# Performance work log

Measured on AMD Instinct MI355X. Metric: run time of the kernel, lower is better.

## Reference

```python
import jax, jax.numpy as jnp
import numpy as np

# dims per init_kwargs / input_specs
N, F_IN, H, C, L = 50000, 128, 128, 40, 4
E = 800000
ALPHA = 0.1   # args.beta -> self.alpha (initial-residual strength)
LAMDA = 0.5   # identity-mapping decay


def setup_inputs() -> dict:
    key = jax.random.key(0)
    ks = jax.random.split(key, 6)
    x = jax.random.normal(ks[0], (N, F_IN), jnp.float32)
    edge_index = jax.random.randint(ks[1], (2, E), 0, N, dtype=jnp.int32)
    s = 1.0 / np.sqrt(H)
    W_in = jax.random.uniform(ks[2], (F_IN, H), jnp.float32, -s, s)
    b_in = jnp.zeros((H,), jnp.float32)
    W_layers = jax.random.uniform(ks[3], (L, H, H), jnp.float32, -s, s)
    W_out = jax.random.uniform(ks[4], (H, C), jnp.float32, -s, s)
    b_out = jnp.zeros((C,), jnp.float32)
    return dict(x=x, edge_index=edge_index, W_in=W_in, b_in=b_in,
                W_layers=W_layers, W_out=W_out, b_out=b_out)


def _gcn_norm(edge_index, n):
    """Symmetric GCN normalization with added self-loops (gcn_norm)."""
    loops = jnp.arange(n, dtype=edge_index.dtype)
    row = jnp.concatenate([edge_index[0], loops])  # destination
    col = jnp.concatenate([edge_index[1], loops])  # source
    deg = jax.ops.segment_sum(jnp.ones(row.shape, jnp.float32), row, num_segments=n)
    dinv = jnp.where(deg > 0, jax.lax.rsqrt(jnp.maximum(deg, 1e-12)), 0.0)
    return row, col, dinv[row] * dinv[col]  # per-edge norm coefficient


def reference(x, edge_index, W_in, b_in, W_layers, W_out, b_out):
    n = x.shape[0]
    row, col, norm = _gcn_norm(edge_index, n)
    # input linear + relu (dropout is identity in eval / p=0)
    h = jax.nn.relu(x @ W_in + b_in)
    h0 = h  # _hidden[0], the initial residual
    # beta_i = log(lamda/(i+1) + 1)
    betas = jnp.log(LAMDA / jnp.arange(1, L + 1, dtype=jnp.float32) + 1.0)

    def layer(h, wb):
        W, beta = wb
        # sparse graph conv: gather-source, scale, scatter-add to dest  [E,H] msgs
        agg = jax.ops.segment_sum(h[col] * norm[:, None], row, num_segments=n)
        support = (1.0 - ALPHA) * agg + ALPHA * h0
        out = beta * (support @ W) + (1.0 - beta) * support  # ((1-b)I + bW)
        return jax.nn.relu(out), None

    h, _ = jax.lax.scan(layer, h, (W_layers, betas))
    return h @ W_out + b_out
```

## Files before the change

### kernel.cpp

```cpp
#include <hip/hip_runtime.h>
#include <hip/hip_bf16.h>
#include <hip/hip_fp16.h>
#include <math.h>

typedef short short8 __attribute__((ext_vector_type(8)));
typedef _Float16 half8 __attribute__((ext_vector_type(8)));
typedef float f32x4  __attribute__((ext_vector_type(4)));

__device__ __forceinline__ unsigned short f2h(float f) {
    return __half_as_ushort(__float2half(f));
}
__device__ __forceinline__ float h2f(unsigned short u) {
    return __half2float(__ushort_as_half(u));
}


__global__ void k_count(const int* __restrict__ dst, int* __restrict__ cnt,
                        unsigned short* __restrict__ rank, int E) {
    int e = blockIdx.x * 256 + threadIdx.x;
    if (e < E) rank[e] = (unsigned short)atomicAdd(&cnt[dst[e]], 1);
}

__global__ void k_scan_part(const int* __restrict__ cnt, int* __restrict__ offs,
                            int* __restrict__ parts, float* __restrict__ dinv, int n) {
    __shared__ int s[256];
    int i = blockIdx.x * 256 + threadIdx.x;
    int v = (i < n) ? cnt[i] : 0;
    s[threadIdx.x] = v;
    __syncthreads();
    #pragma unroll
    for (int d = 1; d < 256; d <<= 1) {
        int t = (threadIdx.x >= d) ? s[threadIdx.x - d] : 0;
        __syncthreads();
        s[threadIdx.x] += t;
        __syncthreads();
    }
    if (i < n) {
        offs[i] = s[threadIdx.x] - v;
        dinv[i] = rsqrtf((float)v + 1.0f);
    }
    if (threadIdx.x == 255) parts[blockIdx.x] = s[255];
}

__global__ void k_scan_tops(int* __restrict__ parts, int np) {
    __shared__ int s[256];
    int tid = threadIdx.x;
    int v = (tid < np) ? parts[tid] : 0;
    s[tid] = v;
    __syncthreads();
    #pragma unroll
    for (int d = 1; d < 256; d <<= 1) {
        int t = (tid >= d) ? s[tid - d] : 0;
        __syncthreads();
        s[tid] += t;
        __syncthreads();
    }
    if (tid < np) parts[tid] = s[tid] - v;
}

__global__ void k_scan_add(int* __restrict__ offs, const int* __restrict__ parts,
                           int n, int e_total) {
    int i = blockIdx.x * 256 + threadIdx.x;
    if (i < n) offs[i] += parts[blockIdx.x];
    if (blockIdx.x == 0 && threadIdx.x == 0) offs[n] = e_total;
}

__global__ void k_scatter(const int* __restrict__ dst, const int* __restrict__ src,
                          const unsigned short* __restrict__ rank,
                          const int* __restrict__ offs,
                          const float* __restrict__ dinv,
                          unsigned* __restrict__ csr, int E) {
    int e = blockIdx.x * 256 + threadIdx.x;
    if (e < E) {
        int d = dst[e], s = src[e];
        float w = 0.9f * dinv[d] * dinv[s];
        csr[offs[d] + (int)rank[e]] = ((unsigned)f2h(w) << 16) | (unsigned)s;
    }
}


__global__ void k_wprep(const float* __restrict__ Wl, const float* __restrict__ Win,
                        const float* __restrict__ Wout,
                        unsigned short* __restrict__ wt,
                        unsigned short* __restrict__ wint,
                        unsigned short* __restrict__ wot, int C) {
    int m = blockIdx.x;
    if (m < 4) {
        for (int i = threadIdx.x; i < 16384; i += 256) {
            int n = i >> 7, k = i & 127;
            wt[m * 16384 + n * 128 + k] = f2h(Wl[m * 16384 + k * 128 + n]);
        }
    } else if (m == 4) {
        for (int i = threadIdx.x; i < 16384; i += 256) {
            int n = i >> 7, k = i & 127;
            wint[n * 128 + k] = f2h(Win[k * 128 + n]);
        }
    } else {
        for (int i = threadIdx.x; i < 48 * 128; i += 256) {
            int n = i >> 7, k = i & 127;
            wot[n * 128 + k] = (n < C) ? f2h(Wout[k * C + n]) : (unsigned short)0;
        }
    }
}


__global__ __launch_bounds__(256)
void k_spmm(const int* __restrict__ offs, const unsigned* __restrict__ csr,
            const unsigned short* __restrict__ hb,
            const unsigned short* __restrict__ h0b,
            const float* __restrict__ dinv,
            unsigned short* __restrict__ supb, int n, int E) {
    int node = blockIdx.x * 8 + (threadIdx.x >> 5);
    if (node >= n) return;
    int l32 = threadIdx.x & 31;
    float di = dinv[node];
    float ws = 0.9f * di * di;
    uint2 sv = *(const uint2*)&hb [((size_t)node << 7) + (l32 << 2)];
    uint2 rv = *(const uint2*)&h0b[((size_t)node << 7) + (l32 << 2)];
    float ax = ws * h2f((unsigned short)(sv.x & 0xffffu)) + 0.1f * h2f((unsigned short)(rv.x & 0xffffu));
    float ay = ws * h2f((unsigned short)(sv.x >> 16))     + 0.1f * h2f((unsigned short)(rv.x >> 16));
    float az = ws * h2f((unsigned short)(sv.y & 0xffffu)) + 0.1f * h2f((unsigned short)(rv.y & 0xffffu));
    float aw = ws * h2f((unsigned short)(sv.y >> 16))     + 0.1f * h2f((unsigned short)(rv.y >> 16));
    int e = offs[node], end = offs[node + 1];
    while (e < end) {
        int nb = end - e;
        if (nb > 32) nb = 32;
        unsigned ce = csr[min(e + l32, E - 1)];
        int i = 0;
        for (; i + 16 <= nb; i += 16) {
            uint2 g[16]; float wv[16];
            #pragma unroll
            for (int j = 0; j < 16; ++j) {
                unsigned u = __shfl(ce, i + j, 32);
                wv[j] = h2f((unsigned short)(u >> 16));
                g[j] = *(const uint2*)&hb[((size_t)(u & 0xffffu) << 7) + (l32 << 2)];
            }
            #pragma unroll
            for (int j = 0; j < 16; ++j) {
                ax += wv[j] * h2f((unsigned short)(g[j].x & 0xffffu));
                ay += wv[j] * h2f((unsigned short)(g[j].x >> 16));
                az += wv[j] * h2f((unsigned short)(g[j].y & 0xffffu));
                aw += wv[j] * h2f((unsigned short)(g[j].y >> 16));
            }
        }
        for (; i + 8 <= nb; i += 8) {
            uint2 g[8]; float wv[8];
            #pragma unroll
            for (int j = 0; j < 8; ++j) {
                unsigned u = __shfl(ce, i + j, 32);
                wv[j] = h2f((unsigned short)(u >> 16));
                g[j] = *(const uint2*)&hb[((size_t)(u & 0xffffu) << 7) + (l32 << 2)];
            }
            #pragma unroll
            for (int j = 0; j < 8; ++j) {
                ax += wv[j] * h2f((unsigned short)(g[j].x & 0xffffu));
                ay += wv[j] * h2f((unsigned short)(g[j].x >> 16));
                az += wv[j] * h2f((unsigned short)(g[j].y & 0xffffu));
                aw += wv[j] * h2f((unsigned short)(g[j].y >> 16));
            }
        }
        for (; i + 4 <= nb; i += 4) {
            uint2 g[4]; float wv[4];
            #pragma unroll
            for (int j = 0; j < 4; ++j) {
                unsigned u = __shfl(ce, i + j, 32);
                wv[j] = h2f((unsigned short)(u >> 16));
                g[j] = *(const uint2*)&hb[((size_t)(u & 0xffffu) << 7) + (l32 << 2)];
            }
            #pragma unroll
            for (int j = 0; j < 4; ++j) {
                ax += wv[j] * h2f((unsigned short)(g[j].x & 0xffffu));
                ay += wv[j] * h2f((unsigned short)(g[j].x >> 16));
                az += wv[j] * h2f((unsigned short)(g[j].y & 0xffffu));
                aw += wv[j] * h2f((unsigned short)(g[j].y >> 16));
            }
        }
        for (; i + 2 <= nb; i += 2) {
            uint2 g[2]; float wv[2];
            #pragma unroll
            for (int j = 0; j < 2; ++j) {
                unsigned u = __shfl(ce, i + j, 32);
                wv[j] = h2f((unsigned short)(u >> 16));
                g[j] = *(const uint2*)&hb[((size_t)(u & 0xffffu) << 7) + (l32 << 2)];
            }
            #pragma unroll
            for (int j = 0; j < 2; ++j) {
                ax += wv[j] * h2f((unsigned short)(g[j].x & 0xffffu));
                ay += wv[j] * h2f((unsigned short)(g[j].x >> 16));
                az += wv[j] * h2f((unsigned short)(g[j].y & 0xffffu));
                aw += wv[j] * h2f((unsigned short)(g[j].y >> 16));
            }
        }
        for (; i < nb; ++i) {
            unsigned u = __shfl(ce, i, 32);
            float w = h2f((unsigned short)(u >> 16));
            uint2 g = *(const uint2*)&hb[((size_t)(u & 0xffffu) << 7) + (l32 << 2)];
            ax += w * h2f((unsigned short)(g.x & 0xffffu));
            ay += w * h2f((unsigned short)(g.x >> 16));
            az += w * h2f((unsigned short)(g.y & 0xffffu));
            aw += w * h2f((unsigned short)(g.y >> 16));
        }
        e += nb;
    }
    uint2 o;
    o.x = (unsigned)f2h(ax) | ((unsigned)f2h(ay) << 16);
    o.y = (unsigned)f2h(az) | ((unsigned)f2h(aw) << 16);
    *(uint2*)&supb[((size_t)node << 7) + (l32 << 2)] = o;
}


__global__ __launch_bounds__(256)
void gemm_in(const float* __restrict__ inA,
             const unsigned short* __restrict__ Bh,
             const float* __restrict__ bias,
             unsigned short* __restrict__ hb,
             unsigned short* __restrict__ h0b, int M) {
    extern __shared__ char lds[];
    char* Ah = lds;
    char* Wh = Ah + 16384;

    const int tid  = threadIdx.x;
    const int row0 = blockIdx.x * 64;

    for (int c = tid; c < 1024; c += 256) {
        int row = c >> 4, k8 = c & 15;
        int grow = row0 + row;
        short8 hv = {0,0,0,0,0,0,0,0};
        if (grow < M) {
            const float* s = &inA[(size_t)grow * 128 + k8 * 8];
            float4 f0 = *(const float4*)s;
            float4 f1 = *(const float4*)(s + 4);
            float ff[8] = {f0.x, f0.y, f0.z, f0.w, f1.x, f1.y, f1.z, f1.w};
            #pragma unroll
            for (int j = 0; j < 8; ++j) hv[j] = (short)f2h(ff[j]);
        }
        *(short8*)(Ah + row * 256 + ((k8 ^ (row & 7)) << 4)) = hv;
    }
    for (int c = tid; c < 2048; c += 256) {
        int n = c >> 4, k8 = c & 15;
        *(short8*)(Wh + n * 256 + ((k8 ^ (n & 7)) << 4)) = *(const short8*)&Bh[n * 128 + k8 * 8];
    }
    __syncthreads();

    const int lane = tid & 63;
    const int w    = tid >> 6;
    const int lr   = lane & 15;
    const int lg   = lane >> 4;

    f32x4 acc[4][2];
    #pragma unroll
    for (int m = 0; m < 4; ++m)
        #pragma unroll
        for (int n2 = 0; n2 < 2; ++n2) acc[m][n2] = (f32x4){0.f, 0.f, 0.f, 0.f};

    #pragma unroll
    for (int kk = 0; kk < 4; ++kk) {
        int k8 = kk * 4 + lg;
        half8 a[4], b[2];
        #pragma unroll
        for (int m = 0; m < 4; ++m) {
            int row = m * 16 + lr;
            a[m] = *(const half8*)(Ah + row * 256 + ((k8 ^ (row & 7)) << 4));
        }
        #pragma unroll
        for (int n2 = 0; n2 < 2; ++n2) {
            int n = (w * 2 + n2) * 16 + lr;
            b[n2] = *(const half8*)(Wh + n * 256 + ((k8 ^ (n & 7)) << 4));
        }
        #pragma unroll
        for (int m = 0; m < 4; ++m)
            #pragma unroll
            for (int n2 = 0; n2 < 2; ++n2)
                acc[m][n2] = __builtin_amdgcn_mfma_f32_16x16x32_f16(a[m], b[n2], acc[m][n2], 0, 0, 0);
    }

    #pragma unroll
    for (int m = 0; m < 4; ++m) {
        #pragma unroll
        for (int n2 = 0; n2 < 2; ++n2) {
            int col = (w * 2 + n2) * 16 + lr;
            #pragma unroll
            for (int r = 0; r < 4; ++r) {
                int row = row0 + m * 16 + lg * 4 + r;
                if (row < M) {
                    float o = fmaxf(acc[m][n2][r] + bias[col], 0.f);
                    unsigned short ob = f2h(o);
                    hb [(size_t)row * 128 + col] = ob;
                    h0b[(size_t)row * 128 + col] = ob;
                }
            }
        }
    }
}


__global__ __launch_bounds__(256)
void gemm_layer(const unsigned short* __restrict__ supb,
                const unsigned short* __restrict__ Bh,
                float beta, float gamma,
                unsigned short* __restrict__ outh, int M) {
    extern __shared__ char lds[];
    char* Ah = lds;
    char* Wh = Ah + 16384;

    const int tid  = threadIdx.x;
    const int row0 = blockIdx.x * 64;

    for (int c = tid; c < 1024; c += 256) {
        int row = c >> 4, k8 = c & 15;
        int grow = row0 + row;
        short8 hv = {0,0,0,0,0,0,0,0};
        if (grow < M) hv = *(const short8*)&supb[(size_t)grow * 128 + k8 * 8];
        *(short8*)(Ah + row * 256 + ((k8 ^ (row & 7)) << 4)) = hv;
    }
    for (int c = tid; c < 2048; c += 256) {
        int n = c >> 4, k8 = c & 15;
        *(short8*)(Wh + n * 256 + ((k8 ^ (n & 7)) << 4)) = *(const short8*)&Bh[n * 128 + k8 * 8];
    }
    __syncthreads();

    const int lane = tid & 63;
    const int w    = tid >> 6;
    const int lr   = lane & 15;
    const int lg   = lane >> 4;

    f32x4 acc[4][2];
    #pragma unroll
    for (int m = 0; m < 4; ++m)
        #pragma unroll
        for (int n2 = 0; n2 < 2; ++n2) acc[m][n2] = (f32x4){0.f, 0.f, 0.f, 0.f};

    #pragma unroll
    for (int kk = 0; kk < 4; ++kk) {
        int k8 = kk * 4 + lg;
        half8 a[4], b[2];
        #pragma unroll
        for (int m = 0; m < 4; ++m) {
            int row = m * 16 + lr;
            a[m] = *(const half8*)(Ah + row * 256 + ((k8 ^ (row & 7)) << 4));
        }
        #pragma unroll
        for (int n2 = 0; n2 < 2; ++n2) {
            int n = (w * 2 + n2) * 16 + lr;
            b[n2] = *(const half8*)(Wh + n * 256 + ((k8 ^ (n & 7)) << 4));
        }
        #pragma unroll
        for (int m = 0; m < 4; ++m)
            #pragma unroll
            for (int n2 = 0; n2 < 2; ++n2)
                acc[m][n2] = __builtin_amdgcn_mfma_f32_16x16x32_f16(a[m], b[n2], acc[m][n2], 0, 0, 0);
    }

    #pragma unroll
    for (int m = 0; m < 4; ++m) {
        #pragma unroll
        for (int n2 = 0; n2 < 2; ++n2) {
            int col = (w * 2 + n2) * 16 + lr;
            int k8c = col >> 3;
            int ebc = (col & 7) * 2;
            #pragma unroll
            for (int r = 0; r < 4; ++r) {
                int rl  = m * 16 + lg * 4 + r;
                int row = row0 + rl;
                if (row < M) {
                    unsigned short rb = *(const unsigned short*)
                        (Ah + rl * 256 + ((k8c ^ (rl & 7)) << 4) + ebc);
                    float o = beta * acc[m][n2][r] + gamma * h2f(rb);
                    o = fmaxf(o, 0.f);
                    outh[(size_t)row * 128 + col] = f2h(o);
                }
            }
        }
    }
}


__global__ __launch_bounds__(256)
void k_out(const unsigned short* __restrict__ hb,
           const unsigned short* __restrict__ Wot,
           const float* __restrict__ bias,
           float* __restrict__ out, int M, int C) {
    extern __shared__ char lds[];
    char* Ah = lds;
    char* Wh = Ah + 16384;

    const int tid  = threadIdx.x;
    const int row0 = blockIdx.x * 64;

    for (int c = tid; c < 1024; c += 256) {
        int row = c >> 4, k8 = c & 15;
        int grow = row0 + row;
        short8 hv = {0,0,0,0,0,0,0,0};
        if (grow < M) hv = *(const short8*)&hb[(size_t)grow * 128 + k8 * 8];
        *(short8*)(Ah + row * 256 + ((k8 ^ (row & 7)) << 4)) = hv;
    }
    for (int c = tid; c < 768; c += 256) {
        int n = c >> 4, k8 = c & 15;
        *(short8*)(Wh + n * 256 + ((k8 ^ (n & 7)) << 4)) = *(const short8*)&Wot[n * 128 + k8 * 8];
    }
    __syncthreads();

    const int lane = tid & 63;
    const int w    = tid >> 6;
    const int lr   = lane & 15;
    const int lg   = lane >> 4;

    f32x4 acc[3];
    #pragma unroll
    for (int n2 = 0; n2 < 3; ++n2) acc[n2] = (f32x4){0.f, 0.f, 0.f, 0.f};

    #pragma unroll
    for (int kk = 0; kk < 4; ++kk) {
        int k8 = kk * 4 + lg;
        int row = w * 16 + lr;
        half8 a = *(const half8*)(Ah + row * 256 + ((k8 ^ (row & 7)) << 4));
        #pragma unroll
        for (int n2 = 0; n2 < 3; ++n2) {
            int n = n2 * 16 + lr;
            half8 b = *(const half8*)(Wh + n * 256 + ((k8 ^ (n & 7)) << 4));
            acc[n2] = __builtin_amdgcn_mfma_f32_16x16x32_f16(a, b, acc[n2], 0, 0, 0);
        }
    }

    #pragma unroll
    for (int n2 = 0; n2 < 3; ++n2) {
        int col = n2 * 16 + lr;
        if (col < C) {
            float bb = bias[col];
            #pragma unroll
            for (int r = 0; r < 4; ++r) {
                int row = row0 + w * 16 + lg * 4 + r;
                if (row < M) out[(size_t)row * C + col] = acc[n2][r] + bb;
            }
        }
    }
}


extern "C" void kernel_launch(void* const* d_in, const int* in_sizes, int n_in,
                              void* d_out, int out_size, void* d_ws, size_t ws_size,
                              hipStream_t stream) {
    const float* x        = (const float*)d_in[0];
    const int*   ei       = (const int*)d_in[1];
    const float* W_in     = (const float*)d_in[2];
    const float* b_in     = (const float*)d_in[3];
    const float* W_layers = (const float*)d_in[4];
    const float* W_out    = (const float*)d_in[5];
    const float* b_out    = (const float*)d_in[6];
    float* out = (float*)d_out;

    const int H = 128;
    const int N = in_sizes[0] / H;
    const int E = in_sizes[1] / 2;
    const int L = in_sizes[4] / (H * H);
    const int C = in_sizes[5] / H;

    char* p = (char*)d_ws;
    auto alloc = [&](size_t bytes) {
        char* r = p;
        p += (bytes + 255) & ~(size_t)255;
        return r;
    };
    int*      cnt   = (int*)alloc((size_t)N * 4);
    int*      offs  = (int*)alloc((size_t)(N + 1) * 4);
    int*      parts = (int*)alloc(256 * 4);
    unsigned* csr   = (unsigned*)alloc((size_t)E * 4);
    unsigned short* rank = (unsigned short*)alloc((size_t)E * 2);
    float*    dinv  = (float*)alloc((size_t)N * 4);
    unsigned short* hb   = (unsigned short*)alloc((size_t)N * H * 2);
    unsigned short* h0b  = (unsigned short*)alloc((size_t)N * H * 2);
    unsigned short* supb = (unsigned short*)alloc((size_t)N * H * 2);
    unsigned short* wt   = (unsigned short*)alloc((size_t)L * H * H * 2);
    unsigned short* wint = (unsigned short*)alloc((size_t)H * H * 2);
    unsigned short* wot  = (unsigned short*)alloc((size_t)48 * H * 2);
    (void)ws_size;

    const int* ei0 = ei;
    const int* ei1 = ei + E;

    const int nblkN = (N + 255) / 256;
    const int nblkE = (E + 255) / 256;

    k_wprep<<<6, 256, 0, stream>>>(W_layers, W_in, W_out, wt, wint, wot, C);

    hipMemsetAsync(cnt, 0, (size_t)N * 4, stream);
    k_count<<<nblkE, 256, 0, stream>>>(ei0, cnt, rank, E);
    k_scan_part<<<nblkN, 256, 0, stream>>>(cnt, offs, parts, dinv, N);
    k_scan_tops<<<1, 256, 0, stream>>>(parts, nblkN);
    k_scan_add<<<nblkN, 256, 0, stream>>>(offs, parts, N, E);
    k_scatter<<<nblkE, 256, 0, stream>>>(ei0, ei1, rank, offs, dinv, csr, E);

    gemm_in<<<(N + 63) / 64, 256, 48 * 1024, stream>>>(x, wint, b_in, hb, h0b, N);

    for (int l = 0; l < L; ++l) {
        float beta = logf(0.5f / (float)(l + 1) + 1.0f);
        k_spmm<<<(N + 7) / 8, 256, 0, stream>>>(offs, csr, hb, h0b, dinv, supb, N, E);
        gemm_layer<<<(N + 63) / 64, 256, 48 * 1024, stream>>>(
            supb, wt + (size_t)l * H * H, beta, 1.0f - beta, hb, N);
    }

    k_out<<<(N + 63) / 64, 256, 28 * 1024, stream>>>(hb, wot, b_out, out, N, C);
}
```

Measured before the change: 294.5 us.

## Split feature dimension into 32-column quarter planes for cache-resident SpMM passes

```diff
diff --git a/kernel.cpp b/kernel.cpp
--- a/kernel.cpp
+++ b/kernel.cpp
@@ -12,6 +12,15 @@
 }
 __device__ __forceinline__ float h2f(unsigned short u) {
     return __half2float(__ushort_as_half(u));
+}
+__device__ __forceinline__ size_t qaddr(int q, int row, int c, int N) {
+    return ((size_t)q * N + row) * 32 + c;
+}
+
+
+__global__ void k_zero(uint4* __restrict__ p, int n16) {
+    int i = blockIdx.x * 256 + threadIdx.x;
+    if (i < n16) p[i] = make_uint4(0u, 0u, 0u, 0u);
 }
 
 
@@ -105,107 +114,95 @@
 
 
 __global__ __launch_bounds__(256)
-void k_spmm(const int* __restrict__ offs, const unsigned* __restrict__ csr,
-            const unsigned short* __restrict__ hb,
-            const unsigned short* __restrict__ h0b,
-            const float* __restrict__ dinv,
-            unsigned short* __restrict__ supb, int n, int E) {
-    int node = blockIdx.x * 8 + (threadIdx.x >> 5);
+void k_spmm_q(const int* __restrict__ offs, const unsigned* __restrict__ csr,
+              const unsigned short* __restrict__ hq,
+              const unsigned short* __restrict__ h0q,
+              const float* __restrict__ dinv,
+              unsigned short* __restrict__ supq,
+              int q, int n, int E) {
+    int node = blockIdx.x * 16 + (threadIdx.x >> 4);
     if (node >= n) return;
-    int l32 = threadIdx.x & 31;
+    int l16 = threadIdx.x & 15;
+    const unsigned short* hqb = hq + (size_t)q * n * 32;
     float di = dinv[node];
     float ws = 0.9f * di * di;
-    uint2 sv = *(const uint2*)&hb [((size_t)node << 7) + (l32 << 2)];
-    uint2 rv = *(const uint2*)&h0b[((size_t)node << 7) + (l32 << 2)];
-    float ax = ws * h2f((unsigned short)(sv.x & 0xffffu)) + 0.1f * h2f((unsigned short)(rv.x & 0xffffu));
-    float ay = ws * h2f((unsigned short)(sv.x >> 16))     + 0.1f * h2f((unsigned short)(rv.x >> 16));
-    float az = ws * h2f((unsigned short)(sv.y & 0xffffu)) + 0.1f * h2f((unsigned short)(rv.y & 0xffffu));
-    float aw = ws * h2f((unsigned short)(sv.y >> 16))     + 0.1f * h2f((unsigned short)(rv.y >> 16));
+    unsigned sv = *(const unsigned*)&hqb[(size_t)node * 32 + l16 * 2];
+    unsigned rv = *(const unsigned*)(h0q + qaddr(q, node, l16 * 2, n));
+    float ax = ws * h2f((unsigned short)(sv & 0xffffu)) + 0.1f * h2f((unsigned short)(rv & 0xffffu));
+    float ay = ws * h2f((unsigned short)(sv >> 16))     + 0.1f * h2f((unsigned short)(rv >> 16));
     int e = offs[node], end = offs[node + 1];
     while (e < end) {
         int nb = end - e;
-        if (nb > 32) nb = 32;
-        unsigned ce = csr[min(e + l32, E - 1)];
+        if (nb > 16) nb = 16;
+        unsigned ce = __builtin_nontemporal_load(&csr[min(e + l16, E - 1)]);
         int i = 0;
         for (; i + 16 <= nb; i += 16) {
-            uint2 g[16]; float wv[16];
+            unsigned g[16]; float wv[16];
             #pragma unroll
             for (int j = 0; j < 16; ++j) {
-                unsigned u = __shfl(ce, i + j, 32);
+                unsigned u = __shfl(ce, i + j, 16);
                 wv[j] = h2f((unsigned short)(u >> 16));
-                g[j] = *(const uint2*)&hb[((size_t)(u & 0xffffu) << 7) + (l32 << 2)];
+                g[j] = *(const unsigned*)&hqb[(size_t)(u & 0xffffu) * 32 + l16 * 2];
             }
             #pragma unroll
             for (int j = 0; j < 16; ++j) {
-                ax += wv[j] * h2f((unsigned short)(g[j].x & 0xffffu));
-                ay += wv[j] * h2f((unsigned short)(g[j].x >> 16));
-                az += wv[j] * h2f((unsigned short)(g[j].y & 0xffffu));
-                aw += wv[j] * h2f((unsigned short)(g[j].y >> 16));
+                ax += wv[j] * h2f((unsigned short)(g[j] & 0xffffu));
+                ay += wv[j] * h2f((unsigned short)(g[j] >> 16));
             }
         }
         for (; i + 8 <= nb; i += 8) {
-            uint2 g[8]; float wv[8];
+            unsigned g[8]; float wv[8];
             #pragma unroll
             for (int j = 0; j < 8; ++j) {
-                unsigned u = __shfl(ce, i + j, 32);
+                unsigned u = __shfl(ce, i + j, 16);
                 wv[j] = h2f((unsigned short)(u >> 16));
-                g[j] = *(const uint2*)&hb[((size_t)(u & 0xffffu) << 7) + (l32 << 2)];
+                g[j] = *(const unsigned*)&hqb[(size_t)(u & 0xffffu) * 32 + l16 * 2];
             }
             #pragma unroll
             for (int j = 0; j < 8; ++j) {
-                ax += wv[j] * h2f((unsigned short)(g[j].x & 0xffffu));
-                ay += wv[j] * h2f((unsigned short)(g[j].x >> 16));
-                az += wv[j] * h2f((unsigned short)(g[j].y & 0xffffu));
-                aw += wv[j] * h2f((unsigned short)(g[j].y >> 16));
+                ax += wv[j] * h2f((unsigned short)(g[j] & 0xffffu));
+                ay += wv[j] * h2f((unsigned short)(g[j] >> 16));
             }
         }
         for (; i + 4 <= nb; i += 4) {
-            uint2 g[4]; float wv[4];
+            unsigned g[4]; float wv[4];
             #pragma unroll
             for (int j = 0; j < 4; ++j) {
-                unsigned u = __shfl(ce, i + j, 32);
+                unsigned u = __shfl(ce, i + j, 16);
                 wv[j] = h2f((unsigned short)(u >> 16));
-                g[j] = *(const uint2*)&hb[((size_t)(u & 0xffffu) << 7) + (l32 << 2)];
+                g[j] = *(const unsigned*)&hqb[(size_t)(u & 0xffffu) * 32 + l16 * 2];
             }
             #pragma unroll
             for (int j = 0; j < 4; ++j) {
-                ax += wv[j] * h2f((unsigned short)(g[j].x & 0xffffu));
-                ay += wv[j] * h2f((unsigned short)(g[j].x >> 16));
-                az += wv[j] * h2f((unsigned short)(g[j].y & 0xffffu));
-                aw += wv[j] * h2f((unsigned short)(g[j].y >> 16));
+                ax += wv[j] * h2f((unsigned short)(g[j] & 0xffffu));
+                ay += wv[j] * h2f((unsigned short)(g[j] >> 16));
             }
         }
         for (; i + 2 <= nb; i += 2) {
-            uint2 g[2]; float wv[2];
+            unsigned g[2]; float wv[2];
             #pragma unroll
             for (int j = 0; j < 2; ++j) {
-                unsigned u = __shfl(ce, i + j, 32);
+                unsigned u = __shfl(ce, i + j, 16);
                 wv[j] = h2f((unsigned short)(u >> 16));
-                g[j] = *(const uint2*)&hb[((size_t)(u & 0xffffu) << 7) + (l32 << 2)];
+                g[j] = *(const unsigned*)&hqb[(size_t)(u & 0xffffu) * 32 + l16 * 2];
             }
             #pragma unroll
             for (int j = 0; j < 2; ++j) {
-                ax += wv[j] * h2f((unsigned short)(g[j].x & 0xffffu));
-                ay += wv[j] * h2f((unsigned short)(g[j].x >> 16));
-                az += wv[j] * h2f((unsigned short)(g[j].y & 0xffffu));
-                aw += wv[j] * h2f((unsigned short)(g[j].y >> 16));
+                ax += wv[j] * h2f((unsigned short)(g[j] & 0xffffu));
+                ay += wv[j] * h2f((unsigned short)(g[j] >> 16));
             }
         }
         for (; i < nb; ++i) {
-            unsigned u = __shfl(ce, i, 32);
+            unsigned u = __shfl(ce, i, 16);
             float w = h2f((unsigned short)(u >> 16));
-            uint2 g = *(const uint2*)&hb[((size_t)(u & 0xffffu) << 7) + (l32 << 2)];
-            ax += w * h2f((unsigned short)(g.x & 0xffffu));
-            ay += w * h2f((unsigned short)(g.x >> 16));
-            az += w * h2f((unsigned short)(g.y & 0xffffu));
-            aw += w * h2f((unsigned short)(g.y >> 16));
+            unsigned g = *(const unsigned*)&hqb[(size_t)(u & 0xffffu) * 32 + l16 * 2];
+            ax += w * h2f((unsigned short)(g & 0xffffu));
+            ay += w * h2f((unsigned short)(g >> 16));
         }
         e += nb;
     }
-    uint2 o;
-    o.x = (unsigned)f2h(ax) | ((unsigned)f2h(ay) << 16);
-    o.y = (unsigned)f2h(az) | ((unsigned)f2h(aw) << 16);
-    *(uint2*)&supb[((size_t)node << 7) + (l32 << 2)] = o;
+    unsigned o = (unsigned)f2h(ax) | ((unsigned)f2h(ay) << 16);
+    __builtin_nontemporal_store(o, (unsigned*)(supq + qaddr(q, node, l16 * 2, n)));
 }
 
 
@@ -213,8 +210,8 @@
 void gemm_in(const float* __restrict__ inA,
              const unsigned short* __restrict__ Bh,
              const float* __restrict__ bias,
-             unsigned short* __restrict__ hb,
-             unsigned short* __restrict__ h0b, int M) {
+             unsigned short* __restrict__ hq,
+             unsigned short* __restrict__ h0q, int M) {
     extern __shared__ char lds[];
     char* Ah = lds;
     char* Wh = Ah + 16384;
@@ -279,14 +276,15 @@
         #pragma unroll
         for (int n2 = 0; n2 < 2; ++n2) {
             int col = (w * 2 + n2) * 16 + lr;
+            int qq = col >> 5, cc = col & 31;
             #pragma unroll
             for (int r = 0; r < 4; ++r) {
                 int row = row0 + m * 16 + lg * 4 + r;
                 if (row < M) {
                     float o = fmaxf(acc[m][n2][r] + bias[col], 0.f);
                     unsigned short ob = f2h(o);
-                    hb [(size_t)row * 128 + col] = ob;
-                    h0b[(size_t)row * 128 + col] = ob;
+                    hq [qaddr(qq, row, cc, M)] = ob;
+                    h0q[qaddr(qq, row, cc, M)] = ob;
                 }
             }
         }
@@ -295,10 +293,10 @@
 
 
 __global__ __launch_bounds__(256)
-void gemm_layer(const unsigned short* __restrict__ supb,
+void gemm_layer(const unsigned short* __restrict__ supq,
                 const unsigned short* __restrict__ Bh,
                 float beta, float gamma,
-                unsigned short* __restrict__ outh, int M) {
+                unsigned short* __restrict__ hq, int M) {
     extern __shared__ char lds[];
     char* Ah = lds;
     char* Wh = Ah + 16384;
@@ -310,7 +308,8 @@
         int row = c >> 4, k8 = c & 15;
         int grow = row0 + row;
         short8 hv = {0,0,0,0,0,0,0,0};
-        if (grow < M) hv = *(const short8*)&supb[(size_t)grow * 128 + k8 * 8];
+        if (grow < M)
+            hv = *(const short8*)&supq[qaddr(k8 >> 2, grow, (k8 & 3) * 8, M)];
         *(short8*)(Ah + row * 256 + ((k8 ^ (row & 7)) << 4)) = hv;
     }
     for (int c = tid; c < 2048; c += 256) {
@@ -356,6 +355,7 @@
         #pragma unroll
         for (int n2 = 0; n2 < 2; ++n2) {
             int col = (w * 2 + n2) * 16 + lr;
+            int qq  = col >> 5, cc = col & 31;
             int k8c = col >> 3;
             int ebc = (col & 7) * 2;
             #pragma unroll
@@ -367,7 +367,7 @@
                         (Ah + rl * 256 + ((k8c ^ (rl & 7)) << 4) + ebc);
                     float o = beta * acc[m][n2][r] + gamma * h2f(rb);
                     o = fmaxf(o, 0.f);
-                    outh[(size_t)row * 128 + col] = f2h(o);
+                    hq[qaddr(qq, row, cc, M)] = f2h(o);
                 }
             }
         }
@@ -376,7 +376,7 @@
 
 
 __global__ __launch_bounds__(256)
-void k_out(const unsigned short* __restrict__ hb,
+void k_out(const unsigned short* __restrict__ hq,
            const unsigned short* __restrict__ Wot,
            const float* __restrict__ bias,
            float* __restrict__ out, int M, int C) {
@@ -391,7 +391,8 @@
         int row = c >> 4, k8 = c & 15;
         int grow = row0 + row;
         short8 hv = {0,0,0,0,0,0,0,0};
-        if (grow < M) hv = *(const short8*)&hb[(size_t)grow * 128 + k8 * 8];
+        if (grow < M)
+            hv = *(const short8*)&hq[qaddr(k8 >> 2, grow, (k8 & 3) * 8, M)];
         *(short8*)(Ah + row * 256 + ((k8 ^ (row & 7)) << 4)) = hv;
     }
     for (int c = tid; c < 768; c += 256) {
@@ -467,9 +468,9 @@
     unsigned* csr   = (unsigned*)alloc((size_t)E * 4);
     unsigned short* rank = (unsigned short*)alloc((size_t)E * 2);
     float*    dinv  = (float*)alloc((size_t)N * 4);
-    unsigned short* hb   = (unsigned short*)alloc((size_t)N * H * 2);
-    unsigned short* h0b  = (unsigned short*)alloc((size_t)N * H * 2);
-    unsigned short* supb = (unsigned short*)alloc((size_t)N * H * 2);
+    unsigned short* hq   = (unsigned short*)alloc((size_t)N * H * 2);
+    unsigned short* h0q  = (unsigned short*)alloc((size_t)N * H * 2);
+    unsigned short* supq = (unsigned short*)alloc((size_t)N * H * 2);
     unsigned short* wt   = (unsigned short*)alloc((size_t)L * H * H * 2);
     unsigned short* wint = (unsigned short*)alloc((size_t)H * H * 2);
     unsigned short* wot  = (unsigned short*)alloc((size_t)48 * H * 2);
@@ -480,24 +481,28 @@
 
     const int nblkN = (N + 255) / 256;
     const int nblkE = (E + 255) / 256;
+    const int n16   = (N + 3) / 4;
 
     k_wprep<<<6, 256, 0, stream>>>(W_layers, W_in, W_out, wt, wint, wot, C);
 
-    hipMemsetAsync(cnt, 0, (size_t)N * 4, stream);
+    k_zero<<<(n16 + 255) / 256, 256, 0, stream>>>((uint4*)cnt, n16);
     k_count<<<nblkE, 256, 0, stream>>>(ei0, cnt, rank, E);
     k_scan_part<<<nblkN, 256, 0, stream>>>(cnt, offs, parts, dinv, N);
     k_scan_tops<<<1, 256, 0, stream>>>(parts, nblkN);
     k_scan_add<<<nblkN, 256, 0, stream>>>(offs, parts, N, E);
     k_scatter<<<nblkE, 256, 0, stream>>>(ei0, ei1, rank, offs, dinv, csr, E);
 
-    gemm_in<<<(N + 63) / 64, 256, 48 * 1024, stream>>>(x, wint, b_in, hb, h0b, N);
-
+    gemm_in<<<(N + 63) / 64, 256, 48 * 1024, stream>>>(x, wint, b_in, hq, h0q, N);
+
+    const int spmm_grid = (N + 15) / 16;
     for (int l = 0; l < L; ++l) {
         float beta = logf(0.5f / (float)(l + 1) + 1.0f);
-        k_spmm<<<(N + 7) / 8, 256, 0, stream>>>(offs, csr, hb, h0b, dinv, supb, N, E);
+        for (int q = 0; q < 4; ++q)
+            k_spmm_q<<<spmm_grid, 256, 0, stream>>>(offs, csr, hq, h0q, dinv,
+                                                    supq, q, N, E);
         gemm_layer<<<(N + 63) / 64, 256, 48 * 1024, stream>>>(
-            supb, wt + (size_t)l * H * H, beta, 1.0f - beta, hb, N);
-    }
-
-    k_out<<<(N + 63) / 64, 256, 28 * 1024, stream>>>(hb, wot, b_out, out, N, C);
-}
+            supq, wt + (size_t)l * H * H, beta, 1.0f - beta, hq, N);
+    }
+
+    k_out<<<(N + 63) / 64, 256, 28 * 1024, stream>>>(hq, wot, b_out, out, N, C);
+}
```

Result: slower. 407.0 us (+38.2%).

## Vectorize edge preprocessing, fold count zeroing into wprep, enlarge layer GEMM tile

Applied to the files above, without the earlier changes.

```diff
diff --git a/kernel.cpp b/kernel.cpp
--- a/kernel.cpp
+++ b/kernel.cpp
@@ -17,8 +17,20 @@
 
 __global__ void k_count(const int* __restrict__ dst, int* __restrict__ cnt,
                         unsigned short* __restrict__ rank, int E) {
-    int e = blockIdx.x * 256 + threadIdx.x;
-    if (e < E) rank[e] = (unsigned short)atomicAdd(&cnt[dst[e]], 1);
+    int t = blockIdx.x * 256 + threadIdx.x;
+    int e = t * 4;
+    if (e + 3 < E) {
+        int4 d = *(const int4*)&dst[e];
+        unsigned r0 = atomicAdd(&cnt[d.x], 1);
+        unsigned r1 = atomicAdd(&cnt[d.y], 1);
+        unsigned r2 = atomicAdd(&cnt[d.z], 1);
+        unsigned r3 = atomicAdd(&cnt[d.w], 1);
+        *(ushort4*)&rank[e] = make_ushort4((unsigned short)r0, (unsigned short)r1,
+                                           (unsigned short)r2, (unsigned short)r3);
+    } else {
+        for (; e < E; ++e)
+            rank[e] = (unsigned short)atomicAdd(&cnt[dst[e]], 1);
+    }
 }
 
 __global__ void k_scan_part(const int* __restrict__ cnt, int* __restrict__ offs,
@@ -70,11 +82,25 @@
                           const int* __restrict__ offs,
                           const float* __restrict__ dinv,
                           unsigned* __restrict__ csr, int E) {
-    int e = blockIdx.x * 256 + threadIdx.x;
-    if (e < E) {
-        int d = dst[e], s = src[e];
-        float w = 0.9f * dinv[d] * dinv[s];
-        csr[offs[d] + (int)rank[e]] = ((unsigned)f2h(w) << 16) | (unsigned)s;
+    int t = blockIdx.x * 256 + threadIdx.x;
+    int e = t * 4;
+    if (e + 3 < E) {
+        int4 d = *(const int4*)&dst[e];
+        int4 s = *(const int4*)&src[e];
+        ushort4 r = *(const ushort4*)&rank[e];
+        float dd0 = dinv[d.x], dd1 = dinv[d.y], dd2 = dinv[d.z], dd3 = dinv[d.w];
+        float ds0 = dinv[s.x], ds1 = dinv[s.y], ds2 = dinv[s.z], ds3 = dinv[s.w];
+        int o0 = offs[d.x], o1 = offs[d.y], o2 = offs[d.z], o3 = offs[d.w];
+        csr[o0 + r.x] = ((unsigned)f2h(0.9f * dd0 * ds0) << 16) | (unsigned)s.x;
+        csr[o1 + r.y] = ((unsigned)f2h(0.9f * dd1 * ds1) << 16) | (unsigned)s.y;
+        csr[o2 + r.z] = ((unsigned)f2h(0.9f * dd2 * ds2) << 16) | (unsigned)s.z;
+        csr[o3 + r.w] = ((unsigned)f2h(0.9f * dd3 * ds3) << 16) | (unsigned)s.w;
+    } else {
+        for (; e < E; ++e) {
+            int d = dst[e], s = src[e];
+            float w = 0.9f * dinv[d] * dinv[s];
+            csr[offs[d] + (int)rank[e]] = ((unsigned)f2h(w) << 16) | (unsigned)s;
+        }
     }
 }
 
@@ -83,7 +109,8 @@
                         const float* __restrict__ Wout,
                         unsigned short* __restrict__ wt,
                         unsigned short* __restrict__ wint,
-                        unsigned short* __restrict__ wot, int C) {
+                        unsigned short* __restrict__ wot, int C,
+                        uint4* __restrict__ cntz, int n16) {
     int m = blockIdx.x;
     if (m < 4) {
         for (int i = threadIdx.x; i < 16384; i += 256) {
@@ -95,11 +122,14 @@
             int n = i >> 7, k = i & 127;
             wint[n * 128 + k] = f2h(Win[k * 128 + n]);
         }
-    } else {
+    } else if (m == 5) {
         for (int i = threadIdx.x; i < 48 * 128; i += 256) {
             int n = i >> 7, k = i & 127;
             wot[n * 128 + k] = (n < C) ? f2h(Wout[k * C + n]) : (unsigned short)0;
         }
+    } else {
+        int i = (m - 6) * 256 + threadIdx.x;
+        if (i < n16) cntz[i] = make_uint4(0u, 0u, 0u, 0u);
     }
 }
 
@@ -294,26 +324,26 @@
 }
 
 
-__global__ __launch_bounds__(256)
+__global__ __launch_bounds__(512)
 void gemm_layer(const unsigned short* __restrict__ supb,
                 const unsigned short* __restrict__ Bh,
                 float beta, float gamma,
                 unsigned short* __restrict__ outh, int M) {
     extern __shared__ char lds[];
     char* Ah = lds;
-    char* Wh = Ah + 16384;
+    char* Wh = Ah + 32768;
 
     const int tid  = threadIdx.x;
-    const int row0 = blockIdx.x * 64;
-
-    for (int c = tid; c < 1024; c += 256) {
+    const int row0 = blockIdx.x * 128;
+
+    for (int c = tid; c < 2048; c += 512) {
         int row = c >> 4, k8 = c & 15;
         int grow = row0 + row;
         short8 hv = {0,0,0,0,0,0,0,0};
         if (grow < M) hv = *(const short8*)&supb[(size_t)grow * 128 + k8 * 8];
         *(short8*)(Ah + row * 256 + ((k8 ^ (row & 7)) << 4)) = hv;
     }
-    for (int c = tid; c < 2048; c += 256) {
+    for (int c = tid; c < 2048; c += 512) {
         int n = c >> 4, k8 = c & 15;
         *(short8*)(Wh + n * 256 + ((k8 ^ (n & 7)) << 4)) = *(const short8*)&Bh[n * 128 + k8 * 8];
     }
@@ -321,46 +351,48 @@
 
     const int lane = tid & 63;
     const int w    = tid >> 6;
+    const int wr   = w >> 1;
+    const int wc   = w & 1;
     const int lr   = lane & 15;
     const int lg   = lane >> 4;
 
-    f32x4 acc[4][2];
-    #pragma unroll
-    for (int m = 0; m < 4; ++m)
-        #pragma unroll
-        for (int n2 = 0; n2 < 2; ++n2) acc[m][n2] = (f32x4){0.f, 0.f, 0.f, 0.f};
+    f32x4 acc[2][4];
+    #pragma unroll
+    for (int m = 0; m < 2; ++m)
+        #pragma unroll
+        for (int n2 = 0; n2 < 4; ++n2) acc[m][n2] = (f32x4){0.f, 0.f, 0.f, 0.f};
 
     #pragma unroll
     for (int kk = 0; kk < 4; ++kk) {
         int k8 = kk * 4 + lg;
-        half8 a[4], b[2];
-        #pragma unroll
-        for (int m = 0; m < 4; ++m) {
-            int row = m * 16 + lr;
+        half8 a[2], b[4];
+        #pragma unroll
+        for (int m = 0; m < 2; ++m) {
+            int row = wr * 32 + m * 16 + lr;
             a[m] = *(const half8*)(Ah + row * 256 + ((k8 ^ (row & 7)) << 4));
         }
         #pragma unroll
-        for (int n2 = 0; n2 < 2; ++n2) {
-            int n = (w * 2 + n2) * 16 + lr;
+        for (int n2 = 0; n2 < 4; ++n2) {
+            int n = wc * 64 + n2 * 16 + lr;
             b[n2] = *(const half8*)(Wh + n * 256 + ((k8 ^ (n & 7)) << 4));
         }
         #pragma unroll
-        for (int m = 0; m < 4; ++m)
-            #pragma unroll
-            for (int n2 = 0; n2 < 2; ++n2)
+        for (int m = 0; m < 2; ++m)
+            #pragma unroll
+            for (int n2 = 0; n2 < 4; ++n2)
                 acc[m][n2] = __builtin_amdgcn_mfma_f32_16x16x32_f16(a[m], b[n2], acc[m][n2], 0, 0, 0);
     }
 
     #pragma unroll
-    for (int m = 0; m < 4; ++m) {
-        #pragma unroll
-        for (int n2 = 0; n2 < 2; ++n2) {
-            int col = (w * 2 + n2) * 16 + lr;
+    for (int m = 0; m < 2; ++m) {
+        #pragma unroll
+        for (int n2 = 0; n2 < 4; ++n2) {
+            int col = wc * 64 + n2 * 16 + lr;
             int k8c = col >> 3;
             int ebc = (col & 7) * 2;
             #pragma unroll
             for (int r = 0; r < 4; ++r) {
-                int rl  = m * 16 + lg * 4 + r;
+                int rl  = wr * 32 + m * 16 + lg * 4 + r;
                 int row = row0 + rl;
                 if (row < M) {
                     unsigned short rb = *(const unsigned short*)
@@ -478,24 +510,26 @@
     const int* ei0 = ei;
     const int* ei1 = ei + E;
 
-    const int nblkN = (N + 255) / 256;
-    const int nblkE = (E + 255) / 256;
-
-    k_wprep<<<6, 256, 0, stream>>>(W_layers, W_in, W_out, wt, wint, wot, C);
-
-    hipMemsetAsync(cnt, 0, (size_t)N * 4, stream);
-    k_count<<<nblkE, 256, 0, stream>>>(ei0, cnt, rank, E);
+    const int nblkN  = (N + 255) / 256;
+    const int nblkE4 = ((E + 3) / 4 + 255) / 256;
+    const int n16    = (N + 3) / 4;
+    const int zblk   = (n16 + 255) / 256;
+
+    k_wprep<<<6 + zblk, 256, 0, stream>>>(W_layers, W_in, W_out, wt, wint, wot, C,
+                                          (uint4*)cnt, n16);
+
+    k_count<<<nblkE4, 256, 0, stream>>>(ei0, cnt, rank, E);
     k_scan_part<<<nblkN, 256, 0, stream>>>(cnt, offs, parts, dinv, N);
     k_scan_tops<<<1, 256, 0, stream>>>(parts, nblkN);
     k_scan_add<<<nblkN, 256, 0, stream>>>(offs, parts, N, E);
-    k_scatter<<<nblkE, 256, 0, stream>>>(ei0, ei1, rank, offs, dinv, csr, E);
+    k_scatter<<<nblkE4, 256, 0, stream>>>(ei0, ei1, rank, offs, dinv, csr, E);
 
     gemm_in<<<(N + 63) / 64, 256, 48 * 1024, stream>>>(x, wint, b_in, hb, h0b, N);
 
     for (int l = 0; l < L; ++l) {
         float beta = logf(0.5f / (float)(l + 1) + 1.0f);
         k_spmm<<<(N + 7) / 8, 256, 0, stream>>>(offs, csr, hb, h0b, dinv, supb, N, E);
-        gemm_layer<<<(N + 63) / 64, 256, 48 * 1024, stream>>>(
+        gemm_layer<<<(N + 127) / 128, 512, 64 * 1024, stream>>>(
             supb, wt + (size_t)l * H * H, beta, 1.0f - beta, hb, N);
     }
 
```

Result: faster. 281.5 us (-4.4%).
